# Kernel tuning notes

Hardware: AMD Instinct MI355X
Metric: run time of the kernel (lower is better)

## Reference

```python
import jax, jax.numpy as jnp
import numpy as np

NEG_INF = -1e9  # same masked_fill constant as the torch module
ALPHA = 0.1     # LeakyReLU negative slope


def setup_inputs() -> dict:
    key = jax.random.key(0)
    k1, k2, k3, k4, k5 = jax.random.split(key, 5)
    B, N, Din, Dout = 8, 2048, 512, 512
    features = jax.random.normal(k1, (B, N, Din), dtype=jnp.float32)
    graph = jax.random.randint(k2, (B, N, N), 0, 2, dtype=jnp.int64)
    # xavier_uniform with gain=1.414: limit = gain*sqrt(6/(fan_in+fan_out))
    lim_w = 1.414 * np.sqrt(6.0 / (Din + Dout))
    w = jax.random.uniform(k3, (Din, Dout), jnp.float32, -lim_w, lim_w)
    lim_a = 1.414 * np.sqrt(6.0 / (Dout + 1))
    a1 = jax.random.uniform(k4, (Dout, 1), jnp.float32, -lim_a, lim_a)
    a2 = jax.random.uniform(k5, (Dout, 1), jnp.float32, -lim_a, lim_a)
    return {"features": features, "graph": graph, "w": w, "a1": a1, "a2": a2}


def reference(features, graph, w, a1, a2):
    # hidden: [B, N, Dout]
    hidden = jnp.einsum("bni,io->bno", features, w)
    s1 = hidden @ a1  # [B, N, 1] -> broadcasts over columns
    s2 = hidden @ a2  # [B, N, 1] -> transposed broadcasts over rows
    # e[b,i,j] = leaky_relu(s1[b,i] + s2[b,j])
    e = jax.nn.leaky_relu(s1 + jnp.swapaxes(s2, 1, 2), negative_slope=ALPHA)
    e = jnp.where(graph == 0, NEG_INF, e)
    attn = jax.nn.softmax(e, axis=-1)  # [B, N, N]; dropout p=0 -> identity
    h_prime = jnp.einsum("bij,bjo->bio", attn, hidden)
    return jax.nn.elu(h_prime)  # concat=True
```

## Files before the change

kernel.cpp:

```cpp
#include <hip/hip_runtime.h>
#include <math.h>

#define B_ 8
#define N_ 2048
#define D_ 512
#define NROWS (B_ * N_)
#define NEG_ALPHA 0.1f

typedef __bf16 bf16;
typedef __bf16 bf16x4 __attribute__((ext_vector_type(4)));
typedef __bf16 bf16x8 __attribute__((ext_vector_type(8)));
typedef float f32x4 __attribute__((ext_vector_type(4)));
typedef float f32x16 __attribute__((ext_vector_type(16)));

__global__ __launch_bounds__(256) void k_prep(const float* __restrict__ W,
                                              bf16* __restrict__ Wt) {
  const int dout = blockIdx.x;
  const int t = threadIdx.x;
#pragma unroll
  for (int p = 0; p < 2; ++p) {
    int din = t + p * 256;
    Wt[dout * D_ + din] = (bf16)W[din * D_ + dout];
  }
}

__global__ __launch_bounds__(256) void k_wa(const float* __restrict__ W,
                                            const float* __restrict__ a1,
                                            const float* __restrict__ a2,
                                            float* __restrict__ wa1,
                                            float* __restrict__ wa2) {
  const int wv = threadIdx.x >> 6, lane = threadIdx.x & 63;
  const int row = blockIdx.x * 4 + wv;
  const float* wr = W + (size_t)row * D_;
  float d1 = 0.f, d2 = 0.f;
#pragma unroll
  for (int p = 0; p < 8; ++p) {
    int c = lane + p * 64;
    float w = wr[c];
    d1 = fmaf(w, a1[c], d1);
    d2 = fmaf(w, a2[c], d2);
  }
#pragma unroll
  for (int off = 32; off > 0; off >>= 1) {
    d1 += __shfl_down(d1, off, 64);
    d2 += __shfl_down(d2, off, 64);
  }
  if (lane == 0) {
    wa1[row] = d1;
    wa2[row] = d2;
  }
}

__global__ __launch_bounds__(256) void k_scores_x(const float* __restrict__ X,
                                                  const float* __restrict__ wa1,
                                                  const float* __restrict__ wa2,
                                                  float* __restrict__ s1,
                                                  float* __restrict__ s2) {
  const int wv = threadIdx.x >> 6, lane = threadIdx.x & 63;
  const int r = blockIdx.x * 4 + wv;
  const float* x = X + (size_t)r * D_;
  float d1 = 0.f, d2 = 0.f;
#pragma unroll
  for (int p = 0; p < 2; ++p) {
    int c = lane * 4 + p * 256;
    float4 xv = *(const float4*)&x[c];
    float4 w1 = *(const float4*)&wa1[c];
    float4 w2 = *(const float4*)&wa2[c];
    d1 += xv.x * w1.x + xv.y * w1.y + xv.z * w1.z + xv.w * w1.w;
    d2 += xv.x * w2.x + xv.y * w2.y + xv.z * w2.z + xv.w * w2.w;
  }
#pragma unroll
  for (int off = 32; off > 0; off >>= 1) {
    d1 += __shfl_down(d1, off, 64);
    d2 += __shfl_down(d2, off, 64);
  }
  if (lane == 0) {
    s1[r] = d1;
    s2[r] = d2;
  }
}

#define LDH 40

__global__ __launch_bounds__(256, 2) void k_hiddenT(const float* __restrict__ X,
                                                    const bf16* __restrict__ Wt,
                                                    bf16* __restrict__ Ht) {
  __shared__ bf16 As[128][LDH];
  __shared__ bf16 Bs[128][LDH];
  const int t = threadIdx.x;
  const int m0 = blockIdx.y * 128;
  const int n0 = blockIdx.x * 128;
  const int lane = t & 63, w = t >> 6;
  const int wm = w >> 1, wn = w & 1;
  const int l15 = lane & 15, q = lane >> 4;

  f32x4 acc[4][4];
#pragma unroll
  for (int i = 0; i < 4; ++i)
#pragma unroll
    for (int j = 0; j < 4; ++j) acc[i][j] = (f32x4){0.f, 0.f, 0.f, 0.f};

  bf16x8 av[2];
  float4 bv[4];
#pragma unroll
  for (int p = 0; p < 2; ++p) {
    int s = t + p * 256;
    av[p] = *(const bf16x8*)&Wt[(size_t)(m0 + (s >> 2)) * D_ + (s & 3) * 8];
  }
#pragma unroll
  for (int p = 0; p < 4; ++p) {
    int s = t + p * 256;
    bv[p] = *(const float4*)&X[(size_t)(n0 + (s >> 3)) * D_ + (s & 7) * 4];
  }

  for (int k0 = 0; k0 < D_; k0 += 32) {
    __syncthreads();
#pragma unroll
    for (int p = 0; p < 2; ++p) {
      int s = t + p * 256;
      *(bf16x8*)&As[s >> 2][(s & 3) * 8] = av[p];
    }
#pragma unroll
    for (int p = 0; p < 4; ++p) {
      int s = t + p * 256;
      float4 v = bv[p];
      bf16x4 h = {(bf16)v.x, (bf16)v.y, (bf16)v.z, (bf16)v.w};
      *(bf16x4*)&Bs[s >> 3][(s & 7) * 4] = h;
    }
    __syncthreads();
    if (k0 + 32 < D_) {
#pragma unroll
      for (int p = 0; p < 2; ++p) {
        int s = t + p * 256;
        av[p] = *(const bf16x8*)&Wt[(size_t)(m0 + (s >> 2)) * D_ + k0 + 32 + (s & 3) * 8];
      }
#pragma unroll
      for (int p = 0; p < 4; ++p) {
        int s = t + p * 256;
        bv[p] = *(const float4*)&X[(size_t)(n0 + (s >> 3)) * D_ + k0 + 32 + (s & 7) * 4];
      }
    }
    bf16x8 a[4], bb[4];
#pragma unroll
    for (int i = 0; i < 4; ++i)
      a[i] = *(const bf16x8*)&As[wm * 64 + i * 16 + l15][q * 8];
#pragma unroll
    for (int j = 0; j < 4; ++j)
      bb[j] = *(const bf16x8*)&Bs[wn * 64 + j * 16 + l15][q * 8];
#pragma unroll
    for (int i = 0; i < 4; ++i)
#pragma unroll
      for (int j = 0; j < 4; ++j)
        acc[i][j] =
            __builtin_amdgcn_mfma_f32_16x16x32_bf16(a[i], bb[j], acc[i][j], 0, 0, 0);
  }
#pragma unroll
  for (int i = 0; i < 4; ++i)
#pragma unroll
    for (int r = 0; r < 4; ++r) {
      int dout = m0 + wm * 64 + i * 16 + q * 4 + r;
#pragma unroll
      for (int j = 0; j < 4; ++j) {
        int row = n0 + wn * 64 + j * 16 + l15;
        Ht[(size_t)dout * NROWS + row] = (bf16)acc[i][j][r];
      }
    }
}

#define AT_BM 64
#define AT_BK 64
#define LDP 72

__global__ __launch_bounds__(512) void k_attn(const bf16* __restrict__ Ht,
                                              const int* __restrict__ graph,
                                              const float* __restrict__ s1,
                                              const float* __restrict__ s2,
                                              float* __restrict__ out) {
  __shared__ __align__(16) bf16 Ps[2][AT_BM][LDP];
  __shared__ float s2s[N_];
  __shared__ float sum_part[AT_BM][8];
  __shared__ float row_sum[AT_BM];

  const int t = threadIdx.x;
  const int bid = blockIdx.x;
  const int b = bid & 7;
  const int i0 = (bid >> 3) * AT_BM;
  const int lane = t & 63, w = t >> 6;
  const int r31 = lane & 31, half = lane >> 5;

  const bf16* Htb = Ht + (size_t)b * N_;
  const int* Gb = graph + ((size_t)b * N_ + i0) * N_;

  for (int c = t; c < N_; c += 512) s2s[c] = s2[b * N_ + c];

  const int pi = t >> 3;
  const int pj = (t & 7) * 8;
  const float s1r = s1[b * N_ + i0 + pi];
  float rsum = 0.f;

  f32x16 acc[2][2];
#pragma unroll
  for (int i = 0; i < 2; ++i)
#pragma unroll
    for (int j = 0; j < 2; ++j)
#pragma unroll
      for (int r = 0; r < 16; ++r) acc[i][j][r] = 0.f;

  int4 g0 = *(const int4*)&Gb[(size_t)pi * N_ + pj];
  int4 g1 = *(const int4*)&Gb[(size_t)pi * N_ + pj + 4];

  __syncthreads();

#pragma unroll 1
  for (int it = 0; it < N_ / AT_BK; ++it) {
    const int j0 = it * AT_BK;
    int jn = j0 + AT_BK;
    if (jn >= N_) jn = 0;
    int4 n0_ = *(const int4*)&Gb[(size_t)pi * N_ + jn + pj];
    int4 n1_ = *(const int4*)&Gb[(size_t)pi * N_ + jn + pj + 4];

    float pv[8];
    {
      int gg[8] = {g0.x, g0.y, g0.z, g0.w, g1.x, g1.y, g1.z, g1.w};
      f32x4 sA = *(const f32x4*)&s2s[j0 + pj];
      f32x4 sB = *(const f32x4*)&s2s[j0 + pj + 4];
      float sv[8] = {sA.x, sA.y, sA.z, sA.w, sB.x, sB.y, sB.z, sB.w};
#pragma unroll
      for (int q = 0; q < 8; ++q) {
        float e = s1r + sv[q];
        e = (e > 0.f) ? e : NEG_ALPHA * e;
        pv[q] = (gg[q] != 0) ? __expf(e) : 0.f;
        rsum += pv[q];
      }
    }
    const int cur = it & 1;
    {
      bf16x8 pb = {(bf16)pv[0], (bf16)pv[1], (bf16)pv[2], (bf16)pv[3],
                   (bf16)pv[4], (bf16)pv[5], (bf16)pv[6], (bf16)pv[7]};
      *(bf16x8*)&Ps[cur][pi][pj] = pb;
    }
    __syncthreads();

    const bf16* Hw0 = Htb + (size_t)(w * 64 + r31) * NROWS + j0;
    const bf16* Hw1 = Htb + (size_t)(w * 64 + 32 + r31) * NROWS + j0;
#pragma unroll
    for (int ks = 0; ks < 4; ++ks) {
      const int ko = ks * 16 + half * 8;
      bf16x8 a0 = *(const bf16x8*)&Ps[cur][r31][ko];
      bf16x8 a1 = *(const bf16x8*)&Ps[cur][32 + r31][ko];
      bf16x8 b0 = *(const bf16x8*)&Hw0[ko];
      bf16x8 b1 = *(const bf16x8*)&Hw1[ko];
      acc[0][0] = __builtin_amdgcn_mfma_f32_32x32x16_bf16(a0, b0, acc[0][0], 0, 0, 0);
      acc[0][1] = __builtin_amdgcn_mfma_f32_32x32x16_bf16(a0, b1, acc[0][1], 0, 0, 0);
      acc[1][0] = __builtin_amdgcn_mfma_f32_32x32x16_bf16(a1, b0, acc[1][0], 0, 0, 0);
      acc[1][1] = __builtin_amdgcn_mfma_f32_32x32x16_bf16(a1, b1, acc[1][1], 0, 0, 0);
    }
    g0 = n0_;
    g1 = n1_;
  }

  sum_part[pi][t & 7] = rsum;
  __syncthreads();
  if (t < AT_BM) {
    float s = 0.f;
#pragma unroll
    for (int k = 0; k < 8; ++k) s += sum_part[t][k];
    row_sum[t] = s;
  }
  __syncthreads();

#pragma unroll
  for (int mt = 0; mt < 2; ++mt) {
    float inv[16];
#pragma unroll
    for (int r = 0; r < 16; ++r)
      inv[r] = 1.f / row_sum[mt * 32 + (r & 3) + 8 * (r >> 2) + 4 * half];
#pragma unroll
    for (int nt = 0; nt < 2; ++nt) {
      const int d = w * 64 + nt * 32 + r31;
#pragma unroll
      for (int r = 0; r < 16; ++r) {
        int i = mt * 32 + (r & 3) + 8 * (r >> 2) + 4 * half;
        float x = acc[mt][nt][r] * inv[r];
        out[((size_t)b * N_ + i0 + i) * D_ + d] = (x > 0.f) ? x : expm1f(x);
      }
    }
  }
}

extern "C" void kernel_launch(void* const* d_in, const int* in_sizes, int n_in,
                              void* d_out, int out_size, void* d_ws,
                              size_t ws_size, hipStream_t stream) {
  const float* X = (const float*)d_in[0];
  const int* graph = (const int*)d_in[1];
  const float* W = (const float*)d_in[2];
  const float* a1 = (const float*)d_in[3];
  const float* a2 = (const float*)d_in[4];
  float* out = (float*)d_out;

  char* ws = (char*)d_ws;
  bf16* Wt = (bf16*)ws;
  bf16* Ht = (bf16*)(ws + (1 << 19));
  float* s1 = (float*)(ws + (1 << 19) + (16 << 20));
  float* s2 = s1 + NROWS;
  float* wa1 = s2 + NROWS;
  float* wa2 = wa1 + D_;

  hipLaunchKernelGGL(k_prep, dim3(512), dim3(256), 0, stream, W, Wt);
  hipLaunchKernelGGL(k_wa, dim3(128), dim3(256), 0, stream, W, a1, a2, wa1, wa2);
  hipLaunchKernelGGL(k_scores_x, dim3(NROWS / 4), dim3(256), 0, stream, X, wa1,
                     wa2, s1, s2);
  hipLaunchKernelGGL(k_hiddenT, dim3(NROWS / 128, D_ / 128), dim3(256), 0,
                     stream, X, Wt, Ht);
  hipLaunchKernelGGL(k_attn, dim3(N_ / AT_BM * B_), dim3(512), 0, stream, Ht,
                     graph, s1, s2, out);
}
```

Measured before the change: 300.7 us.

## Store hidden in MFMA-fragment layout and double-buffer B-operand and graph prefetch

The hidden-transpose GEMM now writes its output in a blocked layout that matches the 32x32x16 MFMA B-fragment, so each lane in the attention kernel reads one contiguous 16-byte chunk per fragment instead of strided rows. The attention loop is unrolled by two with ping-pong register buffers that prefetch the next tile's hidden fragments and the graph mask two iterations ahead. The goal is to remove uncoalesced global loads and hide load latency behind the MFMA work. The cost is more register pressure in a 512-thread kernel and scattered 2-byte stores in the GEMM epilogue.

```diff
diff --git a/kernel.cpp b/kernel.cpp
--- a/kernel.cpp
+++ b/kernel.cpp
@@ -12,6 +12,8 @@
 typedef __bf16 bf16x8 __attribute__((ext_vector_type(8)));
 typedef float f32x4 __attribute__((ext_vector_type(4)));
 typedef float f32x16 __attribute__((ext_vector_type(16)));
+
+#define HTB_BATCH ((D_ / 32) * (N_ / 16) * 512)
 
 __global__ __launch_bounds__(256) void k_prep(const float* __restrict__ W,
                                               bf16* __restrict__ Wt) {
@@ -84,7 +86,7 @@
 
 __global__ __launch_bounds__(256, 2) void k_hiddenT(const float* __restrict__ X,
                                                     const bf16* __restrict__ Wt,
-                                                    bf16* __restrict__ Ht) {
+                                                    bf16* __restrict__ HtB) {
   __shared__ bf16 As[128][LDH];
   __shared__ bf16 Bs[128][LDH];
   const int t = threadIdx.x;
@@ -162,7 +164,14 @@
 #pragma unroll
       for (int j = 0; j < 4; ++j) {
         int row = n0 + wn * 64 + j * 16 + l15;
-        Ht[(size_t)dout * NROWS + row] = (bf16)acc[i][j][r];
+        int bb_ = row >> 11;
+        int jj = row & (N_ - 1);
+        size_t addr = (size_t)bb_ * HTB_BATCH +
+                      ((size_t)((dout >> 5) * (N_ / 16) + (jj >> 4)) * 64 +
+                       ((jj >> 3) & 1) * 32 + (dout & 31)) *
+                          8 +
+                      (jj & 7);
+        HtB[addr] = (bf16)acc[i][j][r];
       }
     }
 }
@@ -170,8 +179,60 @@
 #define AT_BM 64
 #define AT_BK 64
 #define LDP 72
-
-__global__ __launch_bounds__(512) void k_attn(const bf16* __restrict__ Ht,
+#define NIT (N_ / AT_BK)
+
+#define ATTN_BODY(PS, BC, BN, G0, G1, IT)                                      \
+  {                                                                            \
+    const int j0_ = (IT)*AT_BK;                                                \
+    int gg[8] = {G0.x, G0.y, G0.z, G0.w, G1.x, G1.y, G1.z, G1.w};              \
+    {           \
+      int itn = (IT) + 2;                                                      \
+      int jg = (itn < NIT) ? itn * AT_BK : 0;                                  \
+      G0 = *(const int4*)&Gb[(size_t)pi * N_ + jg + pj];                       \
+      G1 = *(const int4*)&Gb[(size_t)pi * N_ + jg + pj + 4];                   \
+    }                                                                          \
+    float pv[8];                                                               \
+    {                                                                          \
+      f32x4 sA = *(const f32x4*)&s2s[j0_ + pj];                                \
+      f32x4 sB = *(const f32x4*)&s2s[j0_ + pj + 4];                            \
+      float sv[8] = {sA.x, sA.y, sA.z, sA.w, sB.x, sB.y, sB.z, sB.w};          \
+      _Pragma("unroll") for (int q_ = 0; q_ < 8; ++q_) {                       \
+        float e = s1r + sv[q_];                                                \
+        e = (e > 0.f) ? e : NEG_ALPHA * e;                                     \
+        pv[q_] = (gg[q_] != 0) ? __expf(e) : 0.f;                              \
+        rsum += pv[q_];                                                        \
+      }                                                                        \
+    }                                                                          \
+    {                                                                          \
+      bf16x8 pb = {(bf16)pv[0], (bf16)pv[1], (bf16)pv[2], (bf16)pv[3],         \
+                   (bf16)pv[4], (bf16)pv[5], (bf16)pv[6], (bf16)pv[7]};        \
+      *(bf16x8*)&Ps[PS][pi][pj] = pb;                                          \
+    }                                                                          \
+    __syncthreads();            \
+    {               \
+      int j0n = ((IT) + 1 < NIT) ? ((IT) + 1) * AT_BK : 0;                     \
+      _Pragma("unroll") for (int nt = 0; nt < 2; ++nt)                         \
+          _Pragma("unroll") for (int ks = 0; ks < 4; ++ks)                     \
+              BN[nt][ks] = *(const bf16x8*)&Hb[(size_t)((                      \
+                  ((w * 2 + nt) * (N_ / 16) + (j0n >> 4) + ks) * 64 + lane))   \
+                  * 8];                                                        \
+    }                                                                          \
+    _Pragma("unroll") for (int ks = 0; ks < 4; ++ks) {                         \
+      const int ko = ks * 16 + hf * 8;                                         \
+      bf16x8 a0 = *(const bf16x8*)&Ps[PS][r31][ko];                            \
+      bf16x8 a1 = *(const bf16x8*)&Ps[PS][32 + r31][ko];                       \
+      acc[0][0] = __builtin_amdgcn_mfma_f32_32x32x16_bf16(a0, BC[0][ks],       \
+                                                          acc[0][0], 0, 0, 0); \
+      acc[0][1] = __builtin_amdgcn_mfma_f32_32x32x16_bf16(a0, BC[1][ks],       \
+                                                          acc[0][1], 0, 0, 0); \
+      acc[1][0] = __builtin_amdgcn_mfma_f32_32x32x16_bf16(a1, BC[0][ks],       \
+                                                          acc[1][0], 0, 0, 0); \
+      acc[1][1] = __builtin_amdgcn_mfma_f32_32x32x16_bf16(a1, BC[1][ks],       \
+                                                          acc[1][1], 0, 0, 0); \
+    }                                                                          \
+  }
+
+__global__ __launch_bounds__(512) void k_attn(const bf16* __restrict__ HtB,
                                               const int* __restrict__ graph,
                                               const float* __restrict__ s1,
                                               const float* __restrict__ s2,
@@ -186,9 +247,9 @@
   const int b = bid & 7;
   const int i0 = (bid >> 3) * AT_BM;
   const int lane = t & 63, w = t >> 6;
-  const int r31 = lane & 31, half = lane >> 5;
-
-  const bf16* Htb = Ht + (size_t)b * N_;
+  const int r31 = lane & 31, hf = lane >> 5;
+
+  const bf16* Hb = HtB + (size_t)b * HTB_BATCH;
   const int* Gb = graph + ((size_t)b * N_ + i0) * N_;
 
   for (int c = t; c < N_; c += 512) s2s[c] = s2[b * N_ + c];
@@ -206,57 +267,25 @@
 #pragma unroll
       for (int r = 0; r < 16; ++r) acc[i][j][r] = 0.f;
 
-  int4 g0 = *(const int4*)&Gb[(size_t)pi * N_ + pj];
-  int4 g1 = *(const int4*)&Gb[(size_t)pi * N_ + pj + 4];
+  bf16x8 bA[2][4], bB[2][4];
+#pragma unroll
+  for (int nt = 0; nt < 2; ++nt)
+#pragma unroll
+    for (int ks = 0; ks < 4; ++ks)
+      bA[nt][ks] = *(const bf16x8*)&Hb[(size_t)(
+          ((w * 2 + nt) * (N_ / 16) + ks) * 64 + lane) * 8];
+  int4 ga0 = *(const int4*)&Gb[(size_t)pi * N_ + pj];
+  int4 ga1 = *(const int4*)&Gb[(size_t)pi * N_ + pj + 4];
+  int4 gb0 = *(const int4*)&Gb[(size_t)pi * N_ + AT_BK + pj];
+  int4 gb1 = *(const int4*)&Gb[(size_t)pi * N_ + AT_BK + pj + 4];
 
   __syncthreads();
 
 #pragma unroll 1
-  for (int it = 0; it < N_ / AT_BK; ++it) {
-    const int j0 = it * AT_BK;
-    int jn = j0 + AT_BK;
-    if (jn >= N_) jn = 0;
-    int4 n0_ = *(const int4*)&Gb[(size_t)pi * N_ + jn + pj];
-    int4 n1_ = *(const int4*)&Gb[(size_t)pi * N_ + jn + pj + 4];
-
-    float pv[8];
-    {
-      int gg[8] = {g0.x, g0.y, g0.z, g0.w, g1.x, g1.y, g1.z, g1.w};
-      f32x4 sA = *(const f32x4*)&s2s[j0 + pj];
-      f32x4 sB = *(const f32x4*)&s2s[j0 + pj + 4];
-      float sv[8] = {sA.x, sA.y, sA.z, sA.w, sB.x, sB.y, sB.z, sB.w};
-#pragma unroll
-      for (int q = 0; q < 8; ++q) {
-        float e = s1r + sv[q];
-        e = (e > 0.f) ? e : NEG_ALPHA * e;
-        pv[q] = (gg[q] != 0) ? __expf(e) : 0.f;
-        rsum += pv[q];
-      }
-    }
-    const int cur = it & 1;
-    {
-      bf16x8 pb = {(bf16)pv[0], (bf16)pv[1], (bf16)pv[2], (bf16)pv[3],
-                   (bf16)pv[4], (bf16)pv[5], (bf16)pv[6], (bf16)pv[7]};
-      *(bf16x8*)&Ps[cur][pi][pj] = pb;
-    }
-    __syncthreads();
-
-    const bf16* Hw0 = Htb + (size_t)(w * 64 + r31) * NROWS + j0;
-    const bf16* Hw1 = Htb + (size_t)(w * 64 + 32 + r31) * NROWS + j0;
-#pragma unroll
-    for (int ks = 0; ks < 4; ++ks) {
-      const int ko = ks * 16 + half * 8;
-      bf16x8 a0 = *(const bf16x8*)&Ps[cur][r31][ko];
-      bf16x8 a1 = *(const bf16x8*)&Ps[cur][32 + r31][ko];
-      bf16x8 b0 = *(const bf16x8*)&Hw0[ko];
-      bf16x8 b1 = *(const bf16x8*)&Hw1[ko];
-      acc[0][0] = __builtin_amdgcn_mfma_f32_32x32x16_bf16(a0, b0, acc[0][0], 0, 0, 0);
-      acc[0][1] = __builtin_amdgcn_mfma_f32_32x32x16_bf16(a0, b1, acc[0][1], 0, 0, 0);
-      acc[1][0] = __builtin_amdgcn_mfma_f32_32x32x16_bf16(a1, b0, acc[1][0], 0, 0, 0);
-      acc[1][1] = __builtin_amdgcn_mfma_f32_32x32x16_bf16(a1, b1, acc[1][1], 0, 0, 0);
-    }
-    g0 = n0_;
-    g1 = n1_;
+  for (int i2 = 0; i2 < NIT / 2; ++i2) {
+    const int it0 = i2 * 2;
+    ATTN_BODY(0, bA, bB, ga0, ga1, it0);
+    ATTN_BODY(1, bB, bA, gb0, gb1, it0 + 1);
   }
 
   sum_part[pi][t & 7] = rsum;
@@ -274,13 +303,13 @@
     float inv[16];
 #pragma unroll
     for (int r = 0; r < 16; ++r)
-      inv[r] = 1.f / row_sum[mt * 32 + (r & 3) + 8 * (r >> 2) + 4 * half];
+      inv[r] = 1.f / row_sum[mt * 32 + (r & 3) + 8 * (r >> 2) + 4 * hf];
 #pragma unroll
     for (int nt = 0; nt < 2; ++nt) {
       const int d = w * 64 + nt * 32 + r31;
 #pragma unroll
       for (int r = 0; r < 16; ++r) {
-        int i = mt * 32 + (r & 3) + 8 * (r >> 2) + 4 * half;
+        int i = mt * 32 + (r & 3) + 8 * (r >> 2) + 4 * hf;
         float x = acc[mt][nt][r] * inv[r];
         out[((size_t)b * N_ + i0 + i) * D_ + d] = (x > 0.f) ? x : expm1f(x);
       }
@@ -300,7 +329,7 @@
 
   char* ws = (char*)d_ws;
   bf16* Wt = (bf16*)ws;
-  bf16* Ht = (bf16*)(ws + (1 << 19));
+  bf16* HtB = (bf16*)(ws + (1 << 19));
   float* s1 = (float*)(ws + (1 << 19) + (16 << 20));
   float* s2 = s1 + NROWS;
   float* wa1 = s2 + NROWS;
@@ -311,7 +340,7 @@
   hipLaunchKernelGGL(k_scores_x, dim3(NROWS / 4), dim3(256), 0, stream, X, wa1,
                      wa2, s1, s2);
   hipLaunchKernelGGL(k_hiddenT, dim3(NROWS / 128, D_ / 128), dim3(256), 0,
-                     stream, X, Wt, Ht);
-  hipLaunchKernelGGL(k_attn, dim3(N_ / AT_BM * B_), dim3(512), 0, stream, Ht,
+                     stream, X, Wt, HtB);
+  hipLaunchKernelGGL(k_attn, dim3(N_ / AT_BM * B_), dim3(512), 0, stream, HtB,
                      graph, s1, s2, out);
 }
```

Measured after the change: 276.6 us. 8.0% less time.
